# Optimization experiments

Measured on AMD Instinct MI355X. Metric: run time of the kernel, lower is better.

Reference implementation:

```python
import jax, jax.numpy as jnp
import numpy as np

N = 8192
D = 768
TEMPERATURE = 0.1
EPS_NORM = 1e-8   # torch CosineSimilarity eps
EPS_LOG = 1e-6


def setup_inputs() -> dict:
    key = jax.random.key(0)
    k1, k2, k3 = jax.random.split(key, 3)
    features = jax.random.normal(k1, (N, D), dtype=jnp.float32)
    positive_mask = jax.random.randint(k2, (N, N), 0, 2).astype(jnp.float32)
    negative_mask = jax.random.randint(k3, (N, N), 0, 2).astype(jnp.float32)
    return {"features": features, "positive_mask": positive_mask, "negative_mask": negative_mask}


def reference(features, positive_mask, negative_mask):
    n = features.shape[0]
    # cosine similarity: normalize then GEMM (same math as broadcasted CosineSimilarity)
    norms = jnp.linalg.norm(features, axis=1, keepdims=True)
    fn = features / jnp.maximum(norms, EPS_NORM)
    sim = jnp.exp(jnp.matmul(fn, fn.T) / TEMPERATURE)  # [N, N]
    # zero out self-contrast on the diagonal of both masks
    not_eye = 1.0 - jnp.eye(n, dtype=features.dtype)
    pm = positive_mask * not_eye
    nm = negative_mask * not_eye
    pos_sums = pm.sum(axis=1)
    pos_sums = jnp.where(pos_sums == 0, 1.0, pos_sums)
    neg = jnp.sum(sim * nm, axis=1, keepdims=True)  # [N, 1]
    log_prob = -jnp.log(sim / neg + EPS_LOG)        # [N, N]
    per_row = jnp.sum(log_prob * pm, axis=1) / pos_sums
    return jnp.mean(per_row)
```

## Files before the change

### kernel.cpp

```cpp
#include <hip/hip_runtime.h>
#include <hip/hip_bf16.h>

#define NROWS 8192
#define DDIM 768

typedef short short8 __attribute__((ext_vector_type(8)));
typedef float floatx4 __attribute__((ext_vector_type(4)));
#define TSTRIDE 132

__global__ __launch_bounds__(256) void normalize_k(const float* __restrict__ f,
                                                   __hip_bfloat16* __restrict__ fn) {
    const int row = blockIdx.x;
    const int t = threadIdx.x;
    const float* fr = f + (size_t)row * DDIM;
    float v0 = fr[t];
    float v1 = fr[t + 256];
    float v2 = fr[t + 512];
    float ss = v0 * v0 + v1 * v1 + v2 * v2;
#pragma unroll
    for (int m = 32; m; m >>= 1) ss += __shfl_xor(ss, m, 64);
    __shared__ float wsum[4];
    if ((t & 63) == 0) wsum[t >> 6] = ss;
    __syncthreads();
    float tot = wsum[0] + wsum[1] + wsum[2] + wsum[3];
    float inv = 1.0f / fmaxf(sqrtf(tot), 1e-8f);
    __hip_bfloat16* o = fn + (size_t)row * DDIM;
    o[t]       = __float2bfloat16(v0 * inv);
    o[t + 256] = __float2bfloat16(v1 * inv);
    o[t + 512] = __float2bfloat16(v2 * inv);
}

__global__ __launch_bounds__(256, 4) void ntxent_main(
        const __hip_bfloat16* __restrict__ fn,
        const float* __restrict__ pmask, const float* __restrict__ nmask,
        float* __restrict__ negG, float* __restrict__ sG,
        float* __restrict__ pG) {
    __shared__ __align__(16) char smem[32 * TSTRIDE * 4];
    __hip_bfloat16* Is = (__hip_bfloat16*)smem;
    __hip_bfloat16* Js = Is + 128 * 32;
    float* T = (float*)smem;

    const int t = threadIdx.x;
    const int lane = t & 63;
    const int wv = t >> 6;
    const int wm = wv & 1;
    const int wn = wv >> 1;
    const int q  = lane >> 4;
    const int cl = lane & 15;

    const int bt = blockIdx.x;
    int r = (int)((sqrtf(8.0f * (float)bt + 1.0f) - 1.0f) * 0.5f);
    while ((r + 1) * (r + 2) / 2 <= bt) ++r;
    while (r * (r + 1) / 2 > bt) --r;
    const int c = bt - r * (r + 1) / 2;
    const int rowBase = c * 128;
    const int colBase = r * 128;
    const bool offDiag = (c != r);

    const int rdSw = ((q ^ ((cl >> 1) & 3)) << 4);

    floatx4 acc[4][4];
#pragma unroll
    for (int mf = 0; mf < 4; ++mf)
#pragma unroll
        for (int nf = 0; nf < 4; ++nf)
            acc[mf][nf] = (floatx4){0.f, 0.f, 0.f, 0.f};

    for (int k0 = 0; k0 < DDIM; k0 += 32) {
        __syncthreads();
#pragma unroll
        for (int it = 0; it < 2; ++it) {
            const int s = it * 256 + t;
            const int rr = s >> 2;
            const int cg = (s & 3) ^ ((rr >> 1) & 3);
            const __hip_bfloat16* ga = fn + (size_t)(rowBase + rr) * DDIM + k0 + cg * 8;
            const __hip_bfloat16* gb = fn + (size_t)(colBase + rr) * DDIM + k0 + cg * 8;
            __builtin_amdgcn_global_load_lds(
                (const __attribute__((address_space(1))) void*)ga,
                (__attribute__((address_space(3))) void*)((char*)Is + s * 16), 16, 0, 0);
            __builtin_amdgcn_global_load_lds(
                (const __attribute__((address_space(1))) void*)gb,
                (__attribute__((address_space(3))) void*)((char*)Js + s * 16), 16, 0, 0);
        }
        __syncthreads();

        short8 jf[4], if_[4];
#pragma unroll
        for (int mf = 0; mf < 4; ++mf) {
            const int rr = wm * 64 + mf * 16 + cl;
            jf[mf] = *(const short8*)((const char*)Js + rr * 64 + rdSw);
        }
#pragma unroll
        for (int nf = 0; nf < 4; ++nf) {
            const int rr = wn * 64 + nf * 16 + cl;
            if_[nf] = *(const short8*)((const char*)Is + rr * 64 + rdSw);
        }
#pragma unroll
        for (int mf = 0; mf < 4; ++mf)
#pragma unroll
            for (int nf = 0; nf < 4; ++nf)
                acc[mf][nf] = __builtin_amdgcn_mfma_f32_16x16x32_bf16(
                    jf[mf], if_[nf], acc[mf][nf], 0, 0, 0);
    }

    const int col64 = colBase + wm * 64;
    const int jb0 = col64 + q * 4;
#pragma unroll
    for (int nf = 0; nf < 4; ++nf) {
        const int grow = rowBase + wn * 64 + nf * 16 + cl;
        const float* prow = pmask + (size_t)grow * NROWS;
        const float* nrow = nmask + (size_t)grow * NROWS;
        float4 pm4[4], nm4[4];
#pragma unroll
        for (int mf = 0; mf < 4; ++mf) {
            pm4[mf] = *(const float4*)(prow + jb0 + mf * 16);
            nm4[mf] = *(const float4*)(nrow + jb0 + mf * 16);
        }
        float aN = 0.f, aS = 0.f, aP = 0.f;
#pragma unroll
        for (int mf = 0; mf < 4; ++mf) {
            const int jbase = jb0 + mf * 16;
#pragma unroll
            for (int reg = 0; reg < 4; ++reg) {
                float pmv = ((const float*)&pm4[mf])[reg];
                float nmv = ((const float*)&nm4[mf])[reg];
                if (grow == jbase + reg) { pmv = 0.f; nmv = 0.f; }
                float v = acc[mf][nf][reg];
                float e = __builtin_amdgcn_exp2f(v * 14.4269504089f);
                aN = fmaf(nmv, e, aN);
                aS = fmaf(pmv, v, aS);
                aP += pmv;
            }
        }
        aN += __shfl_xor(aN, 16, 64);  aN += __shfl_xor(aN, 32, 64);
        aS += __shfl_xor(aS, 16, 64);  aS += __shfl_xor(aS, 32, 64);
        aP += __shfl_xor(aP, 16, 64);  aP += __shfl_xor(aP, 32, 64);
        if (q == 0) {
            atomicAdd(&negG[grow], aN);
            atomicAdd(&sG[grow],   aS);
            atomicAdd(&pG[grow],   aP);
        }
    }

    if (offDiag) {
        const int jl2 = t >> 3;
        const int iseg = (t & 7) * 16;
#pragma unroll
        for (int st = 0; st < 4; ++st) {
            __syncthreads();
            if (wm == (st >> 1)) {
#pragma unroll
                for (int m2 = 0; m2 < 2; ++m2) {
                    const int mf = (st & 1) * 2 + m2;
#pragma unroll
                    for (int nf = 0; nf < 4; ++nf) {
                        const int i = wn * 64 + nf * 16 + cl;
#pragma unroll
                        for (int reg = 0; reg < 4; ++reg) {
                            const int jl = m2 * 16 + q * 4 + reg;
                            T[jl * TSTRIDE + i] = acc[mf][nf][reg];
                        }
                    }
                }
            }
            __syncthreads();
            const int jg = colBase + st * 32 + jl2;
            const float* prow = pmask + (size_t)jg * NROWS + rowBase + iseg;
            const float* nrow = nmask + (size_t)jg * NROWS + rowBase + iseg;
            float4 pm4[4], nm4[4];
#pragma unroll
            for (int u = 0; u < 4; ++u) {
                pm4[u] = *(const float4*)(prow + u * 4);
                nm4[u] = *(const float4*)(nrow + u * 4);
            }
            const float4* tv = (const float4*)(T + jl2 * TSTRIDE + iseg);
            float aN = 0.f, aS = 0.f, aP = 0.f;
#pragma unroll
            for (int u = 0; u < 4; ++u) {
                float4 v4 = tv[u];
#pragma unroll
                for (int e = 0; e < 4; ++e) {
                    float v = ((const float*)&v4)[e];
                    float pmv = ((const float*)&pm4[u])[e];
                    float nmv = ((const float*)&nm4[u])[e];
                    float ex = __builtin_amdgcn_exp2f(v * 14.4269504089f);
                    aN = fmaf(nmv, ex, aN);
                    aS = fmaf(pmv, v, aS);
                    aP += pmv;
                }
            }
            aN += __shfl_xor(aN, 1, 64); aN += __shfl_xor(aN, 2, 64); aN += __shfl_xor(aN, 4, 64);
            aS += __shfl_xor(aS, 1, 64); aS += __shfl_xor(aS, 2, 64); aS += __shfl_xor(aS, 4, 64);
            aP += __shfl_xor(aP, 1, 64); aP += __shfl_xor(aP, 2, 64); aP += __shfl_xor(aP, 4, 64);
            if ((t & 7) == 0) {
                atomicAdd(&negG[jg], aN);
                atomicAdd(&sG[jg],   aS);
                atomicAdd(&pG[jg],   aP);
            }
        }
    }
}

__global__ __launch_bounds__(1024) void final_k(const float* __restrict__ negG,
        const float* __restrict__ sG, const float* __restrict__ pG,
        float* __restrict__ out) {
    const int t = threadIdx.x;
    float sum = 0.f;
    for (int i = t; i < NROWS; i += 1024) {
        float P = pG[i];
        if (P > 0.f) {
            sum += (P * logf(negG[i]) - 10.0f * sG[i]) / P;
        }
    }
#pragma unroll
    for (int m = 32; m; m >>= 1) sum += __shfl_xor(sum, m, 64);
    __shared__ float wsum[16];
    if ((t & 63) == 0) wsum[t >> 6] = sum;
    __syncthreads();
    if (t < 16) {
        float v = wsum[t];
#pragma unroll
        for (int m = 8; m; m >>= 1) v += __shfl_xor(v, m, 16);
        if (t == 0) out[0] = v / (float)NROWS;
    }
}

extern "C" void kernel_launch(void* const* d_in, const int* in_sizes, int n_in,
                              void* d_out, int out_size, void* d_ws, size_t ws_size,
                              hipStream_t stream) {
    const float* feat  = (const float*)d_in[0];
    const float* pmask = (const float*)d_in[1];
    const float* nmask = (const float*)d_in[2];
    float* out = (float*)d_out;

    char* ws = (char*)d_ws;
    __hip_bfloat16* fn = (__hip_bfloat16*)ws;
    float* negG = (float*)(ws + 12582912);
    float* sG = negG + NROWS;
    float* pG = sG + NROWS;

    hipMemsetAsync(negG, 0, 3 * NROWS * sizeof(float), stream);

    normalize_k<<<NROWS, 256, 0, stream>>>(feat, fn);

    ntxent_main<<<2080, 256, 0, stream>>>(fn, pmask, nmask, negG, sG, pG);

    final_k<<<1, 1024, 0, stream>>>(negG, sG, pG, out);
}
```

Measured before the change: 586.1 us.

## Switch cosine-similarity GEMM from bf16 to fp8 MFMA with scaled normalization

Normalized features are scaled by 16 and stored as packed fp8 instead of bf16, which halves the bytes loaded per k-step. The GEMM uses the 16x16x32 fp8 MFMA, and the exp and positive-sum constants are rescaled to undo the factor of 256 in the dot products. The LDS tile layout and swizzle are reworked for 32-byte fp8 rows. This cuts GEMM bandwidth and instruction cost, but fp8 precision may reduce the accuracy of the exp(sim/0.1) terms. The main kernel is likely bound by reading the mask matrices, so the gain may be limited.

```diff
diff --git a/kernel.cpp b/kernel.cpp
--- a/kernel.cpp
+++ b/kernel.cpp
@@ -4,40 +4,42 @@
 #define NROWS 8192
 #define DDIM 768
 
-typedef short short8 __attribute__((ext_vector_type(8)));
 typedef float floatx4 __attribute__((ext_vector_type(4)));
+typedef long i64;
 #define TSTRIDE 132
+#define EK 0.05635527503472514f
+#define SSCALE 0.390625f
 
 __global__ __launch_bounds__(256) void normalize_k(const float* __restrict__ f,
-                                                   __hip_bfloat16* __restrict__ fn) {
+                                                   unsigned char* __restrict__ fn) {
     const int row = blockIdx.x;
     const int t = threadIdx.x;
-    const float* fr = f + (size_t)row * DDIM;
-    float v0 = fr[t];
-    float v1 = fr[t + 256];
-    float v2 = fr[t + 512];
-    float ss = v0 * v0 + v1 * v1 + v2 * v2;
+    const float4* fr4 = (const float4*)(f + (size_t)row * DDIM);
+    float4 v = make_float4(0.f, 0.f, 0.f, 0.f);
+    if (t < 192) v = fr4[t];
+    float ss = v.x * v.x + v.y * v.y + v.z * v.z + v.w * v.w;
 #pragma unroll
     for (int m = 32; m; m >>= 1) ss += __shfl_xor(ss, m, 64);
     __shared__ float wsum[4];
     if ((t & 63) == 0) wsum[t >> 6] = ss;
     __syncthreads();
     float tot = wsum[0] + wsum[1] + wsum[2] + wsum[3];
-    float inv = 1.0f / fmaxf(sqrtf(tot), 1e-8f);
-    __hip_bfloat16* o = fn + (size_t)row * DDIM;
-    o[t]       = __float2bfloat16(v0 * inv);
-    o[t + 256] = __float2bfloat16(v1 * inv);
-    o[t + 512] = __float2bfloat16(v2 * inv);
+    float scale = 16.0f / fmaxf(sqrtf(tot), 1e-8f);
+    if (t < 192) {
+        int w = __builtin_amdgcn_cvt_pk_fp8_f32(v.x * scale, v.y * scale, 0, 0);
+        w = __builtin_amdgcn_cvt_pk_fp8_f32(v.z * scale, v.w * scale, w, 1);
+        ((int*)(fn + (size_t)row * DDIM))[t] = w;
+    }
 }
 
 __global__ __launch_bounds__(256, 4) void ntxent_main(
-        const __hip_bfloat16* __restrict__ fn,
+        const unsigned char* __restrict__ fn,
         const float* __restrict__ pmask, const float* __restrict__ nmask,
         float* __restrict__ negG, float* __restrict__ sG,
         float* __restrict__ pG) {
     __shared__ __align__(16) char smem[32 * TSTRIDE * 4];
-    __hip_bfloat16* Is = (__hip_bfloat16*)smem;
-    __hip_bfloat16* Js = Is + 128 * 32;
+    unsigned char* Is = (unsigned char*)smem;
+    unsigned char* Js = Is + 4096;
     float* T = (float*)smem;
 
     const int t = threadIdx.x;
@@ -57,8 +59,6 @@
     const int colBase = r * 128;
     const bool offDiag = (c != r);
 
-    const int rdSw = ((q ^ ((cl >> 1) & 3)) << 4);
-
     floatx4 acc[4][4];
 #pragma unroll
     for (int mf = 0; mf < 4; ++mf)
@@ -68,38 +68,38 @@
 
     for (int k0 = 0; k0 < DDIM; k0 += 32) {
         __syncthreads();
-#pragma unroll
-        for (int it = 0; it < 2; ++it) {
-            const int s = it * 256 + t;
-            const int rr = s >> 2;
-            const int cg = (s & 3) ^ ((rr >> 1) & 3);
-            const __hip_bfloat16* ga = fn + (size_t)(rowBase + rr) * DDIM + k0 + cg * 8;
-            const __hip_bfloat16* gb = fn + (size_t)(colBase + rr) * DDIM + k0 + cg * 8;
+        {
+            const int row = t >> 1;
+            const int cg = (t & 1) ^ ((row >> 2) & 1);
+            const unsigned char* ga = fn + (size_t)(rowBase + row) * DDIM + k0 + cg * 16;
+            const unsigned char* gb = fn + (size_t)(colBase + row) * DDIM + k0 + cg * 16;
             __builtin_amdgcn_global_load_lds(
                 (const __attribute__((address_space(1))) void*)ga,
-                (__attribute__((address_space(3))) void*)((char*)Is + s * 16), 16, 0, 0);
+                (__attribute__((address_space(3))) void*)(Is + t * 16), 16, 0, 0);
             __builtin_amdgcn_global_load_lds(
                 (const __attribute__((address_space(1))) void*)gb,
-                (__attribute__((address_space(3))) void*)((char*)Js + s * 16), 16, 0, 0);
+                (__attribute__((address_space(3))) void*)(Js + t * 16), 16, 0, 0);
         }
         __syncthreads();
 
-        short8 jf[4], if_[4];
+        i64 jf[4], if_[4];
 #pragma unroll
         for (int mf = 0; mf < 4; ++mf) {
             const int rr = wm * 64 + mf * 16 + cl;
-            jf[mf] = *(const short8*)((const char*)Js + rr * 64 + rdSw);
+            const int off = rr * 32 + ((((q >> 1) ^ ((rr >> 2) & 1))) << 4) + (q & 1) * 8;
+            jf[mf] = *(const i64*)(Js + off);
         }
 #pragma unroll
         for (int nf = 0; nf < 4; ++nf) {
             const int rr = wn * 64 + nf * 16 + cl;
-            if_[nf] = *(const short8*)((const char*)Is + rr * 64 + rdSw);
+            const int off = rr * 32 + ((((q >> 1) ^ ((rr >> 2) & 1))) << 4) + (q & 1) * 8;
+            if_[nf] = *(const i64*)(Is + off);
         }
 #pragma unroll
         for (int mf = 0; mf < 4; ++mf)
 #pragma unroll
             for (int nf = 0; nf < 4; ++nf)
-                acc[mf][nf] = __builtin_amdgcn_mfma_f32_16x16x32_bf16(
+                acc[mf][nf] = __builtin_amdgcn_mfma_f32_16x16x32_fp8_fp8(
                     jf[mf], if_[nf], acc[mf][nf], 0, 0, 0);
     }
 
@@ -126,7 +126,7 @@
                 float nmv = ((const float*)&nm4[mf])[reg];
                 if (grow == jbase + reg) { pmv = 0.f; nmv = 0.f; }
                 float v = acc[mf][nf][reg];
-                float e = __builtin_amdgcn_exp2f(v * 14.4269504089f);
+                float e = __builtin_amdgcn_exp2f(v * EK);
                 aN = fmaf(nmv, e, aN);
                 aS = fmaf(pmv, v, aS);
                 aP += pmv;
@@ -183,7 +183,7 @@
                     float v = ((const float*)&v4)[e];
                     float pmv = ((const float*)&pm4[u])[e];
                     float nmv = ((const float*)&nm4[u])[e];
-                    float ex = __builtin_amdgcn_exp2f(v * 14.4269504089f);
+                    float ex = __builtin_amdgcn_exp2f(v * EK);
                     aN = fmaf(nmv, ex, aN);
                     aS = fmaf(pmv, v, aS);
                     aP += pmv;
@@ -209,7 +209,7 @@
     for (int i = t; i < NROWS; i += 1024) {
         float P = pG[i];
         if (P > 0.f) {
-            sum += (P * logf(negG[i]) - 10.0f * sG[i]) / P;
+            sum += (P * logf(negG[i]) - SSCALE * sG[i]) / P;
         }
     }
 #pragma unroll
@@ -234,8 +234,8 @@
     float* out = (float*)d_out;
 
     char* ws = (char*)d_ws;
-    __hip_bfloat16* fn = (__hip_bfloat16*)ws;
-    float* negG = (float*)(ws + 12582912);
+    unsigned char* fn = (unsigned char*)ws;
+    float* negG = (float*)(ws + 6291456);
     float* sG = negG + NROWS;
     float* pG = sG + NROWS;
 
```

After: 590.6 us. Within noise of the previous version (+0.8%).
